# Kernel tuning notes

Measured on AMD Instinct MI355X. Metric: run time of the kernel, lower is better.

Reference implementation:

```python
import jax, jax.numpy as jnp
import numpy as np
import math

RADIUS = 1.0
PERCENTAGES = (0.02, 0.04, 0.06, 0.08, 0.10)


def _fps(pts, npoint):
    """Furthest point sampling. pts: [N,3] -> idx [npoint] int32 (starts at index 0,
    matching pointnet2 CUDA furthest_point_sample)."""
    N = pts.shape[0]

    def step(carry, _):
        dists, last = carry
        d = jnp.sum((pts - pts[last]) ** 2, axis=-1)
        dists = jnp.minimum(dists, d)
        nxt = jnp.argmax(dists).astype(jnp.int32)
        return (dists, nxt), nxt

    init = (jnp.full((N,), 1e10, pts.dtype), jnp.int32(0))
    _, rest = jax.lax.scan(step, init, None, length=npoint - 1)
    return jnp.concatenate([jnp.zeros((1,), jnp.int32), rest])


def _ball_query(pcd, queries, r, nsample):
    """pcd [B,N,3], queries [B,M,3] -> idx [B,M,nsample] int32.
    First (by index order) points with squared dist < r^2; groups with fewer than
    nsample in-radius points are padded with the first found index (pn2 semantics)."""
    N = pcd.shape[1]
    d2 = jnp.sum((queries[:, :, None, :] - pcd[:, None, :, :]) ** 2, axis=-1)  # [B,M,N]
    key = jnp.where(d2 < r * r, jnp.arange(N, dtype=jnp.int32), jnp.int32(N))
    srt = jnp.sort(key, axis=-1)[:, :, :nsample]  # first in-radius indices
    valid = srt < N
    first = jnp.where(srt[:, :, :1] < N, srt[:, :, :1], 0)
    return jnp.where(valid, srt, first)


def _nn_dist(g):
    """g [G,n,3] -> [G,n] distance to nearest neighbor (2nd-smallest pairwise
    Euclidean distance, i.e. KNN(k=2) dist[:,:,1] including self-distance 0)."""
    sq = jnp.sum(g * g, axis=-1)  # [G,n]
    d2 = sq[:, :, None] + sq[:, None, :] - 2.0 * jnp.einsum('gnc,gmc->gnm', g, g)
    d2 = jnp.maximum(d2, 0.0)
    # safe sqrt (zero grad at exact zeros: self / duplicated padded points)
    d = jnp.where(d2 > 0, jnp.sqrt(jnp.where(d2 > 0, d2, 1.0)), 0.0)
    neg2, _ = jax.lax.top_k(-d, 2)  # two smallest distances
    return -neg2[:, :, 1]


def _uniform_loss(pcd):
    B, N, C = pcd.shape
    npoint = int(N * 0.05)
    fps_idx = jax.vmap(_fps, in_axes=(0, None))(pcd, npoint)  # [B,M]
    new_xyz = jnp.take_along_axis(pcd, fps_idx[:, :, None], axis=1)  # [B,M,3]
    loss = jnp.zeros((), pcd.dtype)
    for p in PERCENTAGES:
        nsample = int(N * p)
        r = math.sqrt(p * RADIUS)
        disk_area = math.pi * RADIUS ** 2 / N
        expect_len = math.sqrt(disk_area)
        idx = _ball_query(pcd, new_xyz, r, nsample)  # [B,M,n]
        grouped = jax.vmap(lambda pts, ii: pts[ii])(pcd, idx)  # [B,M,n,3]
        g = grouped.reshape(B * npoint, nsample, C)
        nn = _nn_dist(g)  # [G,n]
        e_ = 0.1
        u = jnp.abs(nn + e_)
        u = jnp.mean(u, axis=1)  # [G]
        u = (u - expect_len) ** 2 / (expect_len + e_)
        loss = loss + jnp.mean(u) * (p * 100.0) ** 2
    return loss / len(PERCENTAGES)


def setup_inputs() -> dict:
    key = jax.random.key(0)
    pcd = jax.random.uniform(key, (2, 4096, 3), dtype=jnp.float32)
    return {"pcd": pcd}


def reference(pcd):
    return _uniform_loss(pcd)
```

## Files before the change

### kernel.cpp

```cpp
#include <hip/hip_runtime.h>
#include <cmath>

#define NPTS 4096
#define NPOINT 204
#define NPCT 5
#define MAXNS 409
#define FPS_T 256
#define NGROUP 408
#define NPART (NGROUP * NPCT)
#define MAXSLOT 7

#define NWORK  510
#define NROUND 4

#define SMEM_BYTES 65600
#define KEYS_OFF   65536
#define WRES_OFF   6544
#define WTOT_OFF   20880
#define SPART_OFF  20896
#define SQI_OFF    20912

typedef unsigned long long u64;
typedef float f32x2 __attribute__((ext_vector_type(2)));

struct LossParams {
    int   nsample[NPCT];
    float r2[NPCT];
    float wscale[NPCT];
    float expect_len;
};

template <int CTRL>
__device__ __forceinline__ int dpp_imax(int v) {
    int t = __builtin_amdgcn_update_dpp(0, v, CTRL, 0xf, 0xf, true);
    return v > t ? v : t;
}
template <int CTRL>
__device__ __forceinline__ int dpp_imin(int v) {
    int t = __builtin_amdgcn_update_dpp(0x7fffffff, v, CTRL, 0xf, 0xf, false);
    return v < t ? v : t;
}
__device__ __forceinline__ int wave_max_i(int v) {
    v = dpp_imax<0x111>(v); v = dpp_imax<0x112>(v);
    v = dpp_imax<0x114>(v); v = dpp_imax<0x118>(v);
    v = dpp_imax<0x142>(v); v = dpp_imax<0x143>(v);
    return __builtin_amdgcn_readlane(v, 63);
}
__device__ __forceinline__ int wave_min_i(int v) {
    v = dpp_imin<0x111>(v); v = dpp_imin<0x112>(v);
    v = dpp_imin<0x114>(v); v = dpp_imin<0x118>(v);
    v = dpp_imin<0x142>(v); v = dpp_imin<0x143>(v);
    return __builtin_amdgcn_readlane(v, 63);
}
template <int CTRL>
__device__ __forceinline__ u64 dpp_u64max(u64 v) {
    int lo = (int)(unsigned)v;
    int hi = (int)(unsigned)(v >> 32);
    unsigned slo = (unsigned)__builtin_amdgcn_update_dpp(0, lo, CTRL, 0xf, 0xf, true);
    unsigned shi = (unsigned)__builtin_amdgcn_update_dpp(0, hi, CTRL, 0xf, 0xf, true);
    u64 o = ((u64)shi << 32) | slo;
    return v > o ? v : o;
}

__device__ void fps_role(const float* __restrict__ pcd,
                         int* __restrict__ fps_idx,
                         char* smem) {
#pragma clang fp contract(off)
    __builtin_amdgcn_s_setprio(3);
    float4* pts = reinterpret_cast<float4*>(smem);
    u64 (*keys)[4] = reinterpret_cast<u64 (*)[4]>(smem + KEYS_OFF);

    const int b = blockIdx.x;
    const int t = threadIdx.x;
    const int wave = t >> 6, lane = t & 63;
    const float* base = pcd + (size_t)b * NPTS * 3;

    f32x2 X[8], Y[8], Z[8], D[8];
    #pragma unroll
    for (int q = 0; q < 8; ++q) {
        int n0 = (2 * q) * FPS_T + t;
        int n1 = (2 * q + 1) * FPS_T + t;
        float x0 = base[3 * n0 + 0], y0 = base[3 * n0 + 1], z0 = base[3 * n0 + 2];
        float x1 = base[3 * n1 + 0], y1 = base[3 * n1 + 1], z1 = base[3 * n1 + 2];
        pts[n0] = make_float4(x0, y0, z0, 0.0f);
        pts[n1] = make_float4(x1, y1, z1, 0.0f);
        X[q] = (f32x2){x0, x1};
        Y[q] = (f32x2){y0, y1};
        Z[q] = (f32x2){z0, z1};
        D[q] = (f32x2){1e10f, 1e10f};
    }
    int* out = fps_idx + b * NPOINT;
    if (t == 0)
        __hip_atomic_store(&out[0], 0, __ATOMIC_RELAXED, __HIP_MEMORY_SCOPE_AGENT);
    __syncthreads();

    float4 c = pts[0];
    for (int it = 1; it < NPOINT; ++it) {
        f32x2 cxx = (f32x2){c.x, c.x};
        f32x2 cyy = (f32x2){c.y, c.y};
        f32x2 czz = (f32x2){c.z, c.z};
        int bb = -1, bi = 0;
        #pragma unroll
        for (int q = 0; q < 8; ++q) {
            f32x2 dx = X[q] - cxx, dy = Y[q] - cyy, dz = Z[q] - czz;
            f32x2 d  = (dx * dx + dy * dy) + dz * dz;
            f32x2 dd = D[q];
            float d0 = fminf(dd.x, d.x);
            float d1 = fminf(dd.y, d.y);
            D[q] = (f32x2){d0, d1};
            int b0 = __float_as_int(d0);
            int b1 = __float_as_int(d1);
            if (b0 > bb) { bb = b0; bi = (2 * q) * FPS_T + t; }
            if (b1 > bb) { bb = b1; bi = (2 * q + 1) * FPS_T + t; }
        }
        int wmax = wave_max_i(bb);
        int cand = (bb == wmax) ? bi : 0x7fffffff;
        int widx = wave_min_i(cand);
        if (lane == 0)
            keys[it & 1][wave] =
                ((u64)(unsigned)wmax << 32) | (unsigned)~(unsigned)widx;
        asm volatile("s_waitcnt lgkmcnt(0)" ::: "memory");
        __builtin_amdgcn_s_barrier();
        u64 kv = keys[it & 1][lane & 3];
        kv = dpp_u64max<0x111>(kv);
        kv = dpp_u64max<0x112>(kv);
        unsigned lo3 = (unsigned)__builtin_amdgcn_readlane((int)(unsigned)kv, 3);
        int last = (int)~lo3;
        c = pts[last];
        if (t == 0)
            __hip_atomic_store(&out[it], last, __ATOMIC_RELAXED, __HIP_MEMORY_SCOPE_AGENT);
    }
}

template <int K>
__device__ __forceinline__ void phaseB(const float4* __restrict__ gpts,
                                       float2 (*wres)[64],
                                       int j0, int j1, int lane, int cntB) {
    float4 pi[K];
    float m1[K], m2[K];
    #pragma unroll
    for (int s = 0; s < K; ++s) {
        int idx = s * 64 + lane;
        pi[s] = gpts[idx < cntB ? idx : 0];
        m1[s] = 1e30f; m2[s] = 1e30f;
    }
    #pragma unroll 2
    for (int j = j0; j < j1; ++j) {
        float4 a = gpts[j];
        #pragma unroll
        for (int s = 0; s < K; ++s) {
            float tt = pi[s].x * a.x;
            tt = fmaf(pi[s].y, a.y, tt);
            tt = fmaf(pi[s].z, a.z, tt);
            float h = fmaf(-2.0f, tt, a.w);
            m2[s] = __builtin_amdgcn_fmed3f(m1[s], m2[s], h);
            m1[s] = fminf(m1[s], h);
        }
    }
    #pragma unroll
    for (int s = 0; s < K; ++s) wres[s][lane] = (float2){m1[s], m2[s]};
}

__device__ void worker_role(const float* __restrict__ pcd,
                            int* __restrict__ fps_idx,
                            float* __restrict__ partials,
                            const LossParams& P, char* smem) {
    float4* gpts = reinterpret_cast<float4*>(smem);
    auto wres    = reinterpret_cast<float2 (*)[MAXSLOT][64]>(smem + WRES_OFF);
    int*   s_wtot = reinterpret_cast<int*>(smem + WTOT_OFF);
    float* s_part = reinterpret_cast<float*>(smem + SPART_OFF);
    int*   s_qi   = reinterpret_cast<int*>(smem + SQI_OFF);

    const int w = blockIdx.x - 2;
    const int t = threadIdx.x;
    const int wave = t >> 6, lane = t & 63;

    for (int round = 0; round < NROUND; ++round) {
        const int tau  = w + round * NWORK;
        const int m_   = tau / 10;
        const int rem  = tau - m_ * 10;
        const int b    = rem / 5;
        const int pidx = rem - b * 5;

        const int   ns = P.nsample[pidx];
        const float r2 = P.r2[pidx];
        const float* base = pcd + (size_t)b * NPTS * 3;

        if (t == 0) {
            int q;
            while ((q = __hip_atomic_load(&fps_idx[b * NPOINT + m_],
                                          __ATOMIC_RELAXED,
                                          __HIP_MEMORY_SCOPE_AGENT)) < 0)
                __builtin_amdgcn_s_sleep(16);
            s_qi[0] = q;
        }
        __syncthreads();
        const int qi = s_qi[0];
        float qx = base[3 * qi + 0], qy = base[3 * qi + 1], qz = base[3 * qi + 2];

        unsigned long long msk[16];
        int lbase[16];
        int run = 0;
        #pragma unroll 4
        for (int s = 0; s < 16; ++s) {
            int n = wave * 1024 + s * 64 + lane;
            float x = base[3 * n + 0];
            float y = base[3 * n + 1];
            float z = base[3 * n + 2];
            float d2;
            {
#pragma clang fp contract(off)
                float dx = qx - x, dy = qy - y, dz = qz - z;
                float aa = dx * dx, bb2 = dy * dy, cc = dz * dz;
                d2 = (aa + bb2) + cc;
            }
            msk[s] = __ballot(d2 < r2);
            lbase[s] = run;
            run += __popcll(msk[s]);
        }
        if (lane == 0) s_wtot[wave] = run;
        __syncthreads();
        int w0 = s_wtot[0], w1 = s_wtot[1], w2 = s_wtot[2], w3 = s_wtot[3];
        int Bw = (wave > 0 ? w0 : 0) + (wave > 1 ? w1 : 0) + (wave > 2 ? w2 : 0);
        int cnt  = w0 + w1 + w2 + w3;
        int cntB = cnt < ns ? cnt : ns;
        const int npad = ns - cntB;

        #pragma unroll 4
        for (int s = 0; s < 16; ++s) {
            int gb = Bw + lbase[s];
            if (gb >= ns) break;
            unsigned long long mk = msk[s];
            bool in = (mk >> lane) & 1ull;
            int pos = gb + __popcll(mk & ((1ull << lane) - 1ull));
            if (in && pos < ns) {
                int n = wave * 1024 + s * 64 + lane;
                float x = base[3 * n], y = base[3 * n + 1], z = base[3 * n + 2];
                float sq = fmaf(x, x, fmaf(y, y, z * z));
                gpts[pos] = make_float4(x, y, z, sq);
            }
        }
        __syncthreads();

        const int quarter = (cntB + 3) >> 2;
        const int j0 = wave * quarter;
        const int j1 = (j0 + quarter) < cntB ? (j0 + quarter) : cntB;
        const int nslot = (cntB + 63) >> 6;
        switch (nslot) {
            case 1: phaseB<1>(gpts, wres[wave], j0, j1, lane, cntB); break;
            case 2: phaseB<2>(gpts, wres[wave], j0, j1, lane, cntB); break;
            case 3: phaseB<3>(gpts, wres[wave], j0, j1, lane, cntB); break;
            case 4: phaseB<4>(gpts, wres[wave], j0, j1, lane, cntB); break;
            case 5: phaseB<5>(gpts, wres[wave], j0, j1, lane, cntB); break;
            case 6: phaseB<6>(gpts, wres[wave], j0, j1, lane, cntB); break;
            default: phaseB<7>(gpts, wres[wave], j0, j1, lane, cntB); break;
        }
        __syncthreads();

        float sum = 0.0f;
        for (int it = t; it < nslot * 64; it += 256) {
            int i = it;
            if (i < cntB) {
                int s = it >> 6, l = it & 63;
                float2 a  = wres[0][s][l];
                float2 bq = wres[1][s][l];
                float2 cq = wres[2][s][l];
                float2 dq = wres[3][s][l];
                float e1 = fminf(a.x, bq.x), e2 = fminf(fmaxf(a.x, bq.x), fminf(a.y, bq.y));
                float f1 = fminf(cq.x, dq.x), f2 = fminf(fmaxf(cq.x, dq.x), fminf(cq.y, dq.y));
                float m2v = fminf(fmaxf(e1, f1), fminf(e2, f2));
                float sq = gpts[i].w;
                float d2 = fmaxf(sq + m2v, 0.0f);
                if (!(i == 0 && npad > 0)) sum += sqrtf(d2);
            }
        }
        #pragma unroll
        for (int off = 32; off; off >>= 1) sum += __shfl_down(sum, off);
        if (lane == 0) s_part[wave] = sum;
        __syncthreads();
        if (t == 0) {
            float tot = s_part[0] + s_part[1] + s_part[2] + s_part[3] + 0.1f * (float)ns;
            float u  = tot / (float)ns;
            float du = u - P.expect_len;
            partials[tau] = du * du / (P.expect_len + 0.1f) * P.wscale[pidx];
        }
    }
}

__global__ __launch_bounds__(256, 2) void fused_kernel(const float* __restrict__ pcd,
                                                       int* __restrict__ fps_idx,
                                                       float* __restrict__ partials,
                                                       LossParams P) {
    __shared__ __align__(16) char smem[SMEM_BYTES];
    if (blockIdx.x < 2) {
        fps_role(pcd, fps_idx, smem);
    } else {
        worker_role(pcd, fps_idx, partials, P, smem);
    }
}

__global__ __launch_bounds__(256) void reduce_kernel(const float* __restrict__ partials,
                                                     float* __restrict__ out) {
    const int t = threadIdx.x;
    __shared__ float sp[4];
    float s = 0.0f;
    for (int i = t; i < NPART; i += 256) s += partials[i];
    #pragma unroll
    for (int off = 32; off; off >>= 1) s += __shfl_down(s, off);
    if ((t & 63) == 0) sp[t >> 6] = s;
    __syncthreads();
    if (t == 0) out[0] = sp[0] + sp[1] + sp[2] + sp[3];
}

extern "C" void kernel_launch(void* const* d_in, const int* in_sizes, int n_in,
                              void* d_out, int out_size, void* d_ws, size_t ws_size,
                              hipStream_t stream) {
    const float* pcd = (const float*)d_in[0];
    const int B = in_sizes[0] / (NPTS * 3);
    float* out = (float*)d_out;
    int*   fps = (int*)d_ws;
    float* partials = (float*)d_ws + NGROUP;

    hipMemsetAsync(fps, 0xFF, NGROUP * sizeof(int), stream);

    LossParams P;
    const double ps[NPCT] = {0.02, 0.04, 0.06, 0.08, 0.10};
    for (int i = 0; i < NPCT; ++i) {
        P.nsample[i] = (int)(NPTS * ps[i]);
        double r = std::sqrt(ps[i] * 1.0);
        P.r2[i] = (float)(r * r);
        double w = (ps[i] * 100.0) * (ps[i] * 100.0);
        P.wscale[i] = (float)(w / (double)(B * NPOINT * NPCT));
    }
    P.expect_len = (float)std::sqrt(3.14159265358979323846 / (double)NPTS);

    fused_kernel<<<dim3(2 + NWORK), dim3(256), 0, stream>>>(pcd, fps, partials, P);
    reduce_kernel<<<dim3(1), dim3(256), 0, stream>>>(partials, out);
}
```

Before: 187.2 us.

## Widen fused kernel blocks to 512 threads, splitting FPS and worker phases over eight waves

Doubles the block size from 256 to 512 threads, so FPS holds half as many points per thread and the cross-wave argmax reduction gains a third DPP stage over eight wave keys. Worker blocks split ball-query scanning and the pairwise nearest-neighbour phase across eight waves and merge eight partial min-pairs. The aim is to shorten the serial FPS critical path and each group's work. In exchange, every FPS iteration has a barrier across more waves, and the shared-memory layout grows.

```diff
diff --git a/kernel.cpp b/kernel.cpp
--- a/kernel.cpp
+++ b/kernel.cpp
@@ -5,20 +5,21 @@
 #define NPOINT 204
 #define NPCT 5
 #define MAXNS 409
-#define FPS_T 256
+#define FPS_T 512
 #define NGROUP 408
 #define NPART (NGROUP * NPCT)
 #define MAXSLOT 7
+#define NWAVE 8
 
 #define NWORK  510
 #define NROUND 4
 
-#define SMEM_BYTES 65600
+#define SMEM_BYTES 65664
 #define KEYS_OFF   65536
 #define WRES_OFF   6544
-#define WTOT_OFF   20880
-#define SPART_OFF  20896
-#define SQI_OFF    20912
+#define WTOT_OFF   35216
+#define SPART_OFF  35248
+#define SQI_OFF    35280
 
 typedef unsigned long long u64;
 typedef float f32x2 __attribute__((ext_vector_type(2)));
@@ -68,16 +69,16 @@
 #pragma clang fp contract(off)
     __builtin_amdgcn_s_setprio(3);
     float4* pts = reinterpret_cast<float4*>(smem);
-    u64 (*keys)[4] = reinterpret_cast<u64 (*)[4]>(smem + KEYS_OFF);
+    u64 (*keys)[NWAVE] = reinterpret_cast<u64 (*)[NWAVE]>(smem + KEYS_OFF);
 
     const int b = blockIdx.x;
     const int t = threadIdx.x;
     const int wave = t >> 6, lane = t & 63;
     const float* base = pcd + (size_t)b * NPTS * 3;
 
-    f32x2 X[8], Y[8], Z[8], D[8];
+    f32x2 X[4], Y[4], Z[4], D[4];
     #pragma unroll
-    for (int q = 0; q < 8; ++q) {
+    for (int q = 0; q < 4; ++q) {
         int n0 = (2 * q) * FPS_T + t;
         int n1 = (2 * q + 1) * FPS_T + t;
         float x0 = base[3 * n0 + 0], y0 = base[3 * n0 + 1], z0 = base[3 * n0 + 2];
@@ -101,7 +102,7 @@
         f32x2 czz = (f32x2){c.z, c.z};
         int bb = -1, bi = 0;
         #pragma unroll
-        for (int q = 0; q < 8; ++q) {
+        for (int q = 0; q < 4; ++q) {
             f32x2 dx = X[q] - cxx, dy = Y[q] - cyy, dz = Z[q] - czz;
             f32x2 d  = (dx * dx + dy * dy) + dz * dz;
             f32x2 dd = D[q];
@@ -121,11 +122,12 @@
                 ((u64)(unsigned)wmax << 32) | (unsigned)~(unsigned)widx;
         asm volatile("s_waitcnt lgkmcnt(0)" ::: "memory");
         __builtin_amdgcn_s_barrier();
-        u64 kv = keys[it & 1][lane & 3];
+        u64 kv = keys[it & 1][lane & 7];
         kv = dpp_u64max<0x111>(kv);
         kv = dpp_u64max<0x112>(kv);
-        unsigned lo3 = (unsigned)__builtin_amdgcn_readlane((int)(unsigned)kv, 3);
-        int last = (int)~lo3;
+        kv = dpp_u64max<0x114>(kv);
+        unsigned lo7 = (unsigned)__builtin_amdgcn_readlane((int)(unsigned)kv, 7);
+        int last = (int)~lo7;
         c = pts[last];
         if (t == 0)
             __hip_atomic_store(&out[it], last, __ATOMIC_RELAXED, __HIP_MEMORY_SCOPE_AGENT);
@@ -161,6 +163,11 @@
     for (int s = 0; s < K; ++s) wres[s][lane] = (float2){m1[s], m2[s]};
 }
 
+__device__ __forceinline__ float2 min2merge(float2 a, float2 b) {
+    return (float2){fminf(a.x, b.x),
+                    fminf(fmaxf(a.x, b.x), fminf(a.y, b.y))};
+}
+
 __device__ void worker_role(const float* __restrict__ pcd,
                             int* __restrict__ fps_idx,
                             float* __restrict__ partials,
@@ -198,12 +205,12 @@
         const int qi = s_qi[0];
         float qx = base[3 * qi + 0], qy = base[3 * qi + 1], qz = base[3 * qi + 2];
 
-        unsigned long long msk[16];
-        int lbase[16];
+        unsigned long long msk[8];
+        int lbase[8];
         int run = 0;
         #pragma unroll 4
-        for (int s = 0; s < 16; ++s) {
-            int n = wave * 1024 + s * 64 + lane;
+        for (int s = 0; s < 8; ++s) {
+            int n = wave * 512 + s * 64 + lane;
             float x = base[3 * n + 0];
             float y = base[3 * n + 1];
             float z = base[3 * n + 2];
@@ -220,21 +227,25 @@
         }
         if (lane == 0) s_wtot[wave] = run;
         __syncthreads();
-        int w0 = s_wtot[0], w1 = s_wtot[1], w2 = s_wtot[2], w3 = s_wtot[3];
-        int Bw = (wave > 0 ? w0 : 0) + (wave > 1 ? w1 : 0) + (wave > 2 ? w2 : 0);
-        int cnt  = w0 + w1 + w2 + w3;
+        int Bw = 0, cnt = 0;
+        #pragma unroll
+        for (int j = 0; j < NWAVE; ++j) {
+            int wj = s_wtot[j];
+            cnt += wj;
+            if (j < wave) Bw += wj;
+        }
         int cntB = cnt < ns ? cnt : ns;
         const int npad = ns - cntB;
 
         #pragma unroll 4
-        for (int s = 0; s < 16; ++s) {
+        for (int s = 0; s < 8; ++s) {
             int gb = Bw + lbase[s];
             if (gb >= ns) break;
             unsigned long long mk = msk[s];
             bool in = (mk >> lane) & 1ull;
             int pos = gb + __popcll(mk & ((1ull << lane) - 1ull));
             if (in && pos < ns) {
-                int n = wave * 1024 + s * 64 + lane;
+                int n = wave * 512 + s * 64 + lane;
                 float x = base[3 * n], y = base[3 * n + 1], z = base[3 * n + 2];
                 float sq = fmaf(x, x, fmaf(y, y, z * z));
                 gpts[pos] = make_float4(x, y, z, sq);
@@ -242,9 +253,9 @@
         }
         __syncthreads();
 
-        const int quarter = (cntB + 3) >> 2;
-        const int j0 = wave * quarter;
-        const int j1 = (j0 + quarter) < cntB ? (j0 + quarter) : cntB;
+        const int eighth = (cntB + 7) >> 3;
+        const int j0 = wave * eighth;
+        const int j1 = (j0 + eighth) < cntB ? (j0 + eighth) : cntB;
         const int nslot = (cntB + 63) >> 6;
         switch (nslot) {
             case 1: phaseB<1>(gpts, wres[wave], j0, j1, lane, cntB); break;
@@ -258,17 +269,17 @@
         __syncthreads();
 
         float sum = 0.0f;
-        for (int it = t; it < nslot * 64; it += 256) {
+        for (int it = t; it < nslot * 64; it += FPS_T) {
             int i = it;
             if (i < cntB) {
                 int s = it >> 6, l = it & 63;
-                float2 a  = wres[0][s][l];
-                float2 bq = wres[1][s][l];
-                float2 cq = wres[2][s][l];
-                float2 dq = wres[3][s][l];
-                float e1 = fminf(a.x, bq.x), e2 = fminf(fmaxf(a.x, bq.x), fminf(a.y, bq.y));
-                float f1 = fminf(cq.x, dq.x), f2 = fminf(fmaxf(cq.x, dq.x), fminf(cq.y, dq.y));
-                float m2v = fminf(fmaxf(e1, f1), fminf(e2, f2));
+                float2 e  = min2merge(wres[0][s][l], wres[1][s][l]);
+                float2 f  = min2merge(wres[2][s][l], wres[3][s][l]);
+                float2 g  = min2merge(wres[4][s][l], wres[5][s][l]);
+                float2 h  = min2merge(wres[6][s][l], wres[7][s][l]);
+                float2 ef = min2merge(e, f);
+                float2 gh = min2merge(g, h);
+                float m2v = fminf(fmaxf(ef.x, gh.x), fminf(ef.y, gh.y));
                 float sq = gpts[i].w;
                 float d2 = fmaxf(sq + m2v, 0.0f);
                 if (!(i == 0 && npad > 0)) sum += sqrtf(d2);
@@ -279,7 +290,10 @@
         if (lane == 0) s_part[wave] = sum;
         __syncthreads();
         if (t == 0) {
-            float tot = s_part[0] + s_part[1] + s_part[2] + s_part[3] + 0.1f * (float)ns;
+            float tot = 0.0f;
+            #pragma unroll
+            for (int j = 0; j < NWAVE; ++j) tot += s_part[j];
+            tot += 0.1f * (float)ns;
             float u  = tot / (float)ns;
             float du = u - P.expect_len;
             partials[tau] = du * du / (P.expect_len + 0.1f) * P.wscale[pidx];
@@ -287,10 +301,10 @@
     }
 }
 
-__global__ __launch_bounds__(256, 2) void fused_kernel(const float* __restrict__ pcd,
-                                                       int* __restrict__ fps_idx,
-                                                       float* __restrict__ partials,
-                                                       LossParams P) {
+__global__ __launch_bounds__(FPS_T, 4) void fused_kernel(const float* __restrict__ pcd,
+                                                         int* __restrict__ fps_idx,
+                                                         float* __restrict__ partials,
+                                                         LossParams P) {
     __shared__ __align__(16) char smem[SMEM_BYTES];
     if (blockIdx.x < 2) {
         fps_role(pcd, fps_idx, smem);
@@ -334,6 +348,6 @@
     }
     P.expect_len = (float)std::sqrt(3.14159265358979323846 / (double)NPTS);
 
-    fused_kernel<<<dim3(2 + NWORK), dim3(256), 0, stream>>>(pcd, fps, partials, P);
+    fused_kernel<<<dim3(2 + NWORK), dim3(FPS_T), 0, stream>>>(pcd, fps, partials, P);
     reduce_kernel<<<dim3(1), dim3(256), 0, stream>>>(partials, out);
 }
```

Measured after the change: 185.4 us, median of 2. Within noise of the previous version (-1.0%).
